# Kernel tuning notes

Hardware: AMD Instinct MI355X
Metric: run time of the kernel (lower is better)

## Reference

```python
import jax, jax.numpy as jnp
import numpy as np

B, T, D, H = 64, 1024, 512, 512  # batch, time, input_dim, num_units


def setup_inputs() -> dict:
    key = jax.random.key(0)
    k1, k2 = jax.random.split(key)
    x = jax.random.normal(k1, (B, T, D), dtype=jnp.float32)
    # BasicRNNCell kernel: [input_dim + num_units, num_units]
    W = jax.random.normal(k2, (D + H, H), dtype=jnp.float32) * (1.0 / np.sqrt(D + H))
    b = jnp.zeros((H,), dtype=jnp.float32)
    return {"x": x, "W": W, "b": b}


def reference(x, W, b):
    # tf.nn.dynamic_rnn with BasicRNNCell: h_t = tanh([x_t, h_{t-1}] @ W + b)
    Wx = W[:D]   # [D, H] input->hidden
    Wh = W[D:]   # [H, H] hidden->hidden
    # Precompute the input contribution for all timesteps in one big GEMM.
    xw = jnp.einsum('btd,dh->bth', x, Wx) + b  # [B, T, H]

    def step(h, xw_t):
        h_new = jnp.tanh(xw_t + h @ Wh)
        return h_new, h_new

    h0 = jnp.zeros((x.shape[0], H), dtype=x.dtype)
    _, outs = jax.lax.scan(step, h0, jnp.swapaxes(xw, 0, 1))  # outs: [T, B, H]
    return jnp.swapaxes(outs, 0, 1)  # [B, T, H]
```

## Files before the change

kernel.cpp:

```cpp
#include <hip/hip_runtime.h>
#include <math.h>

#define Bb 64
#define Tt 1024
#define Dd 512
#define Hh 512

#define TM 128
#define TN 128
#define TK 16
#define LDP (TN + 4)

__global__ __launch_bounds__(256) void gemm_xw(const float* __restrict__ x,
                                               const float* __restrict__ W,
                                               const float* __restrict__ bias,
                                               float* __restrict__ out) {
    __shared__ float As[TK][LDP];
    __shared__ float Bs[TK][LDP];

    const int tid = threadIdx.x;
    const int m0 = blockIdx.x * TM;
    const int n0 = blockIdx.y * TN;
    const int tx = tid & 15;
    const int ty = tid >> 4;

    float acc[8][8];
    #pragma unroll
    for (int i = 0; i < 8; i++)
        #pragma unroll
        for (int j = 0; j < 8; j++) acc[i][j] = 0.0f;

    for (int k0 = 0; k0 < Dd; k0 += TK) {
        #pragma unroll
        for (int i = 0; i < 2; i++) {
            const int idx = tid * 2 + i;
            const int r = idx >> 2;
            const int c = idx & 3;
            const float4 av = *(const float4*)(x + (size_t)(m0 + r) * Dd + k0 + c * 4);
            As[c * 4 + 0][r] = av.x;
            As[c * 4 + 1][r] = av.y;
            As[c * 4 + 2][r] = av.z;
            As[c * 4 + 3][r] = av.w;
            const int kk = idx >> 5;
            const int cg = (idx & 31) * 4;
            const float4 bv = *(const float4*)(W + (size_t)(k0 + kk) * Hh + n0 + cg);
            *(float4*)(&Bs[kk][cg]) = bv;
        }
        __syncthreads();

        #pragma unroll
        for (int kk = 0; kk < TK; kk++) {
            float a[8], b[8];
            #pragma unroll
            for (int i = 0; i < 8; i++) a[i] = As[kk][ty * 8 + i];
            #pragma unroll
            for (int j = 0; j < 8; j++) b[j] = Bs[kk][tx * 8 + j];
            #pragma unroll
            for (int i = 0; i < 8; i++)
                #pragma unroll
                for (int j = 0; j < 8; j++) acc[i][j] += a[i] * b[j];
        }
        __syncthreads();
    }

    #pragma unroll
    for (int i = 0; i < 8; i++) {
        const size_t row = (size_t)(m0 + ty * 8 + i) * Hh;
        const int n = n0 + tx * 8;
        float4 v0, v1;
        v0.x = acc[i][0] + bias[n + 0];
        v0.y = acc[i][1] + bias[n + 1];
        v0.z = acc[i][2] + bias[n + 2];
        v0.w = acc[i][3] + bias[n + 3];
        v1.x = acc[i][4] + bias[n + 4];
        v1.y = acc[i][5] + bias[n + 5];
        v1.z = acc[i][6] + bias[n + 6];
        v1.w = acc[i][7] + bias[n + 7];
        *(float4*)(out + row + n) = v0;
        *(float4*)(out + row + n + 4) = v1;
    }
}

__device__ unsigned long long g_hbuf[(size_t)Bb * 2 * Hh];

__global__ __launch_bounds__(1024, 4) void scan_rnn(const float* __restrict__ W,
                                                    float* __restrict__ out) {
    const float* __restrict__ Wh = W + (size_t)Dd * Hh;
    const int r = blockIdx.x & 63;
    const int c = blockIdx.x >> 6;
    const int tid = threadIdx.x;
    const int g = tid & 31;
    const int s = tid >> 5;

    float* rowbase = out + (size_t)r * Tt * Hh;
    unsigned long long* hrow = g_hbuf + (size_t)r * 2 * Hh;

    __shared__ float ps[2][32][128];
    __shared__ int sdead;

    float4 w4[16];
    {
        const float4* wbase = (const float4*)(Wh + (size_t)(s * 16) * Hh) + (c * 32 + g);
        #pragma unroll
        for (int kk = 0; kk < 16; kk++) w4[kk] = wbase[(size_t)kk * 128];
    }
    #pragma unroll
    for (int kk = 0; kk < 16; kk++)
        asm volatile("" : "+v"(w4[kk].x), "+v"(w4[kk].y), "+v"(w4[kk].z), "+v"(w4[kk].w));

    float hw[16];
    #pragma unroll
    for (int i = 0; i < 16; i++) hw[i] = 0.0f;

    if (tid == 0) sdead = 0;
    __syncthreads();

    for (int t = 0; t < Tt; t++) {
        float zpre = 0.0f;
        if (tid < 128) zpre = rowbase[(size_t)t * Hh + c * 128 + tid];

        float ax = 0.0f, ay = 0.0f, az = 0.0f, aw = 0.0f;
        #pragma unroll
        for (int q = 0; q < 16; q++) {
            const float h = hw[q];
            const float4 a = w4[q];
            ax += h * a.x; ay += h * a.y; az += h * a.z; aw += h * a.w;
        }
        {
            float4 accv; accv.x = ax; accv.y = ay; accv.z = az; accv.w = aw;
            *(float4*)&ps[t & 1][s][g * 4] = accv;
        }

        __syncthreads();
        const int dead = sdead;

        if (tid < 128) {
            float z = zpre;
            #pragma unroll
            for (int q = 0; q < 32; q++) z += ps[t & 1][q][tid];
            const float hn = tanhf(z);
            if (t < Tt - 1) {
                const unsigned long long pkt =
                    ((unsigned long long)(unsigned)(t + 1) << 32) | __float_as_uint(hn);
                __hip_atomic_store(&hrow[(size_t)(t & 1) * Hh + c * 128 + tid], pkt,
                                   __ATOMIC_RELAXED, __HIP_MEMORY_SCOPE_AGENT);
            }
            rowbase[(size_t)t * Hh + c * 128 + tid] = hn;
        }

        if (t < Tt - 1) {
            float f = 0.0f;
            if (g < 16 && !dead) {
                unsigned long long* src = &hrow[(size_t)(t & 1) * Hh + s * 16 + g];
                const unsigned want = (unsigned)(t + 1);
                unsigned long long v;
                int spins = 0;
                for (;;) {
                    v = __hip_atomic_load(src, __ATOMIC_RELAXED, __HIP_MEMORY_SCOPE_AGENT);
                    if ((unsigned)(v >> 32) == want) break;
                    __builtin_amdgcn_s_sleep(1);
                    if (++spins > (1 << 14)) { sdead = 1; break; }
                }
                f = __uint_as_float((unsigned)v);
            }
            const int base = tid & 32;
            #pragma unroll
            for (int i = 0; i < 16; i++) hw[i] = __shfl(f, base + i, 64);
        }
    }
}

extern "C" void kernel_launch(void* const* d_in, const int* in_sizes, int n_in,
                              void* d_out, int out_size, void* d_ws, size_t ws_size,
                              hipStream_t stream) {
    const float* x = (const float*)d_in[0];
    const float* W = (const float*)d_in[1];
    const float* b = (const float*)d_in[2];
    float* out = (float*)d_out;
    (void)d_ws; (void)ws_size;

    dim3 ggrid((Bb * Tt) / TM, Hh / TN);
    gemm_xw<<<ggrid, dim3(256), 0, stream>>>(x, W, b, out);
    scan_rnn<<<dim3(256), dim3(1024), 0, stream>>>(W, out);
}
```

Baseline: 2.500 ms.

## Interleave two batch rows per block to overlap peer hidden-state waits with compute

Each scan block now handles two batch rows (p and p+32) instead of one, halving the grid to 128 blocks. The recurrent step for one row is computed while otherwise-idle threads spin-poll the cross-block hidden-state packets of the other row, which hides inter-block synchronization latency. Hidden states are staged in shared memory instead of being broadcast by wavefront shuffles, and spinning now busy-waits briefly before sleeping. The cost is four block barriers per step instead of one, plus half as many blocks running in parallel, so each block does twice the matvec work serially.

```diff
diff --git a/kernel.cpp b/kernel.cpp
--- a/kernel.cpp
+++ b/kernel.cpp
@@ -86,16 +86,19 @@
 __global__ __launch_bounds__(1024, 4) void scan_rnn(const float* __restrict__ W,
                                                     float* __restrict__ out) {
     const float* __restrict__ Wh = W + (size_t)Dd * Hh;
-    const int r = blockIdx.x & 63;
-    const int c = blockIdx.x >> 6;
+    const int p = blockIdx.x & 31;
+    const int c = blockIdx.x >> 5;
     const int tid = threadIdx.x;
     const int g = tid & 31;
     const int s = tid >> 5;
 
-    float* rowbase = out + (size_t)r * Tt * Hh;
-    unsigned long long* hrow = g_hbuf + (size_t)r * 2 * Hh;
-
-    __shared__ float ps[2][32][128];
+    float* baseA = out + (size_t)p * Tt * Hh + (size_t)c * 128;
+    float* baseB = out + (size_t)(p + 32) * Tt * Hh + (size_t)c * 128;
+    unsigned long long* hrowA = g_hbuf + (size_t)p * 2 * Hh;
+    unsigned long long* hrowB = g_hbuf + (size_t)(p + 32) * 2 * Hh;
+
+    __shared__ float hsA[Hh], hsB[Hh];
+    __shared__ float psA[32][128], psB[32][128];
     __shared__ int sdead;
 
     float4 w4[16];
@@ -108,65 +111,117 @@
     for (int kk = 0; kk < 16; kk++)
         asm volatile("" : "+v"(w4[kk].x), "+v"(w4[kk].y), "+v"(w4[kk].z), "+v"(w4[kk].w));
 
-    float hw[16];
-    #pragma unroll
-    for (int i = 0; i < 16; i++) hw[i] = 0.0f;
-
+    if (tid < Hh) { hsA[tid] = 0.0f; hsB[tid] = 0.0f; }
     if (tid == 0) sdead = 0;
     __syncthreads();
 
     for (int t = 0; t < Tt; t++) {
-        float zpre = 0.0f;
-        if (tid < 128) zpre = rowbase[(size_t)t * Hh + c * 128 + tid];
-
-        float ax = 0.0f, ay = 0.0f, az = 0.0f, aw = 0.0f;
-        #pragma unroll
-        for (int q = 0; q < 16; q++) {
-            const float h = hw[q];
-            const float4 a = w4[q];
-            ax += h * a.x; ay += h * a.y; az += h * a.z; aw += h * a.w;
-        }
+        float zA = 0.0f, zB = 0.0f;
+        if (tid < 128)      zA = baseA[(size_t)t * Hh + tid];
+        else if (tid < 256) zB = baseB[(size_t)t * Hh + (tid - 128)];
+
         {
-            float4 accv; accv.x = ax; accv.y = ay; accv.z = az; accv.w = aw;
-            *(float4*)&ps[t & 1][s][g * 4] = accv;
-        }
-
-        __syncthreads();
-        const int dead = sdead;
+            float ax = 0.f, ay = 0.f, az = 0.f, aw = 0.f;
+            #pragma unroll
+            for (int kq = 0; kq < 4; kq++) {
+                const float4 hv = *(const float4*)&hsA[s * 16 + kq * 4];
+                const float4 a0 = w4[kq * 4 + 0];
+                const float4 a1 = w4[kq * 4 + 1];
+                const float4 a2 = w4[kq * 4 + 2];
+                const float4 a3 = w4[kq * 4 + 3];
+                ax += hv.x * a0.x; ay += hv.x * a0.y; az += hv.x * a0.z; aw += hv.x * a0.w;
+                ax += hv.y * a1.x; ay += hv.y * a1.y; az += hv.y * a1.z; aw += hv.y * a1.w;
+                ax += hv.z * a2.x; ay += hv.z * a2.y; az += hv.z * a2.z; aw += hv.z * a2.w;
+                ax += hv.w * a3.x; ay += hv.w * a3.y; az += hv.w * a3.z; aw += hv.w * a3.w;
+            }
+            float4 v; v.x = ax; v.y = ay; v.z = az; v.w = aw;
+            *(float4*)&psA[s][g * 4] = v;
+        }
+        __syncthreads();
 
         if (tid < 128) {
-            float z = zpre;
-            #pragma unroll
-            for (int q = 0; q < 32; q++) z += ps[t & 1][q][tid];
+            float z = zA;
+            #pragma unroll
+            for (int q = 0; q < 32; q++) z += psA[q][tid];
             const float hn = tanhf(z);
             if (t < Tt - 1) {
                 const unsigned long long pkt =
                     ((unsigned long long)(unsigned)(t + 1) << 32) | __float_as_uint(hn);
-                __hip_atomic_store(&hrow[(size_t)(t & 1) * Hh + c * 128 + tid], pkt,
+                __hip_atomic_store(&hrowA[(size_t)(t & 1) * Hh + c * 128 + tid], pkt,
                                    __ATOMIC_RELAXED, __HIP_MEMORY_SCOPE_AGENT);
-            }
-            rowbase[(size_t)t * Hh + c * 128 + tid] = hn;
-        }
-
-        if (t < Tt - 1) {
-            float f = 0.0f;
-            if (g < 16 && !dead) {
-                unsigned long long* src = &hrow[(size_t)(t & 1) * Hh + s * 16 + g];
-                const unsigned want = (unsigned)(t + 1);
-                unsigned long long v;
-                int spins = 0;
-                for (;;) {
-                    v = __hip_atomic_load(src, __ATOMIC_RELAXED, __HIP_MEMORY_SCOPE_AGENT);
-                    if ((unsigned)(v >> 32) == want) break;
-                    __builtin_amdgcn_s_sleep(1);
-                    if (++spins > (1 << 14)) { sdead = 1; break; }
-                }
-                f = __uint_as_float((unsigned)v);
-            }
-            const int base = tid & 32;
-            #pragma unroll
-            for (int i = 0; i < 16; i++) hw[i] = __shfl(f, base + i, 64);
-        }
+                hsA[c * 128 + tid] = hn;
+            }
+            baseA[(size_t)t * Hh + tid] = hn;
+        } else if (tid >= 640 && t >= 1 && sdead == 0) {
+            const int idx = tid - 640;
+            const int pp = idx >> 7;
+            const int cp = pp + (pp >= c ? 1 : 0);
+            const int jj = idx & 127;
+            unsigned long long* src = &hrowB[(size_t)((t - 1) & 1) * Hh + cp * 128 + jj];
+            const unsigned want = (unsigned)t;
+            unsigned long long v;
+            int spins = 0;
+            for (;;) {
+                v = __hip_atomic_load(src, __ATOMIC_RELAXED, __HIP_MEMORY_SCOPE_AGENT);
+                if ((unsigned)(v >> 32) == want) break;
+                if (++spins > 64) __builtin_amdgcn_s_sleep(1);
+                if (spins > (1 << 16)) { sdead = 1; break; }
+            }
+            hsB[cp * 128 + jj] = __uint_as_float((unsigned)v);
+        }
+        __syncthreads();
+
+        {
+            float ax = 0.f, ay = 0.f, az = 0.f, aw = 0.f;
+            #pragma unroll
+            for (int kq = 0; kq < 4; kq++) {
+                const float4 hv = *(const float4*)&hsB[s * 16 + kq * 4];
+                const float4 a0 = w4[kq * 4 + 0];
+                const float4 a1 = w4[kq * 4 + 1];
+                const float4 a2 = w4[kq * 4 + 2];
+                const float4 a3 = w4[kq * 4 + 3];
+                ax += hv.x * a0.x; ay += hv.x * a0.y; az += hv.x * a0.z; aw += hv.x * a0.w;
+                ax += hv.y * a1.x; ay += hv.y * a1.y; az += hv.y * a1.z; aw += hv.y * a1.w;
+                ax += hv.z * a2.x; ay += hv.z * a2.y; az += hv.z * a2.z; aw += hv.z * a2.w;
+                ax += hv.w * a3.x; ay += hv.w * a3.y; az += hv.w * a3.z; aw += hv.w * a3.w;
+            }
+            float4 v; v.x = ax; v.y = ay; v.z = az; v.w = aw;
+            *(float4*)&psB[s][g * 4] = v;
+        }
+        __syncthreads();
+
+        if (tid >= 128 && tid < 256) {
+            const int j = tid - 128;
+            float z = zB;
+            #pragma unroll
+            for (int q = 0; q < 32; q++) z += psB[q][j];
+            const float hn = tanhf(z);
+            if (t < Tt - 1) {
+                const unsigned long long pkt =
+                    ((unsigned long long)(unsigned)(t + 1) << 32) | __float_as_uint(hn);
+                __hip_atomic_store(&hrowB[(size_t)(t & 1) * Hh + c * 128 + j], pkt,
+                                   __ATOMIC_RELAXED, __HIP_MEMORY_SCOPE_AGENT);
+                hsB[c * 128 + j] = hn;
+            }
+            baseB[(size_t)t * Hh + j] = hn;
+        } else if (tid >= 256 && tid < 640 && t < Tt - 1 && sdead == 0) {
+            const int idx = tid - 256;
+            const int pp = idx >> 7;
+            const int cp = pp + (pp >= c ? 1 : 0);
+            const int jj = idx & 127;
+            unsigned long long* src = &hrowA[(size_t)(t & 1) * Hh + cp * 128 + jj];
+            const unsigned want = (unsigned)(t + 1);
+            unsigned long long v;
+            int spins = 0;
+            for (;;) {
+                v = __hip_atomic_load(src, __ATOMIC_RELAXED, __HIP_MEMORY_SCOPE_AGENT);
+                if ((unsigned)(v >> 32) == want) break;
+                if (++spins > 64) __builtin_amdgcn_s_sleep(1);
+                if (spins > (1 << 16)) { sdead = 1; break; }
+            }
+            hsA[cp * 128 + jj] = __uint_as_float((unsigned)v);
+        }
+        __syncthreads();
     }
 }
 
@@ -181,5 +236,5 @@
 
     dim3 ggrid((Bb * Tt) / TM, Hh / TN);
     gemm_xw<<<ggrid, dim3(256), 0, stream>>>(x, W, b, out);
-    scan_rnn<<<dim3(256), dim3(1024), 0, stream>>>(W, out);
+    scan_rnn<<<dim3(128), dim3(1024), 0, stream>>>(W, out);
 }
```

Result: faster. 2.376 ms (-5.0%).
